# Optimization experiments

Hardware: AMD Instinct MI355X
Metric: run time of the kernel (lower is better)

The kernel has to match this reference:

```python
import jax, jax.numpy as jnp
import numpy as np

B, C, H, W = 32, 512, 32, 32
CI = C // 2  # inter_channels
EPS = 1e-5


def setup_inputs() -> dict:
    key = jax.random.key(0)
    ks = jax.random.split(key, 12)
    s = 0.02
    return {
        "x": jax.random.normal(ks[0], (B, C, H, W), jnp.float32),
        "w_g": jax.random.normal(ks[1], (CI, C), jnp.float32) * s,
        "b_g": jax.random.normal(ks[2], (CI,), jnp.float32) * s,
        "w_theta": jax.random.normal(ks[3], (CI, C), jnp.float32) * s,
        "b_theta": jax.random.normal(ks[4], (CI,), jnp.float32) * s,
        "w_phi": jax.random.normal(ks[5], (CI, C), jnp.float32) * s,
        "b_phi": jax.random.normal(ks[6], (CI,), jnp.float32) * s,
        "w_W": jax.random.normal(ks[7], (C, CI), jnp.float32) * s,
        "b_W": jax.random.normal(ks[8], (C,), jnp.float32) * s,
        "bn_gamma": jax.random.normal(ks[9], (C,), jnp.float32) * 0.1 + 1.0,
        "bn_beta": jax.random.normal(ks[10], (C,), jnp.float32) * 0.1,
        "bn_mean": jax.random.normal(ks[11], (C,), jnp.float32) * 0.1,
        "bn_var": jnp.abs(jax.random.normal(jax.random.fold_in(key, 99), (C,), jnp.float32)) * 0.5 + 0.5,
    }


def reference(x, w_g, b_g, w_theta, b_theta, w_phi, b_phi, w_W, b_W,
              bn_gamma, bn_beta, bn_mean, bn_var):
    b, c, h, w = x.shape
    n = h * w
    xf = x.reshape(b, c, n)  # [B, C, N]
    # 1x1 convs == per-pixel channel matmuls
    g = jnp.einsum('oc,bcn->bon', w_g, xf) + b_g[:, None]          # [B, Ci, N]
    theta = jnp.einsum('oc,bcn->bon', w_theta, xf) + b_theta[:, None]
    phi = jnp.einsum('oc,bcn->bon', w_phi, xf) + b_phi[:, None]
    # f[b, i, j] = theta_i . phi_j ; scaled by 1/N (softmax-free attention)
    f_div_C = jnp.einsum('bcn,bcm->bnm', theta, phi) / n           # [B, N, N]
    # y[b, c, n] = sum_m f[b, n, m] * g[b, c, m]
    y = jnp.einsum('bnm,bcm->bcn', f_div_C, g)                     # [B, Ci, N]
    # W: 1x1 conv back to C channels + BatchNorm (inference form)
    Wy = jnp.einsum('oi,bin->bon', w_W, y) + b_W[:, None]          # [B, C, N]
    inv_std = jax.lax.rsqrt(bn_var + EPS)
    bn = (Wy - bn_mean[:, None]) * (inv_std * bn_gamma)[:, None] + bn_beta[:, None]
    z = bn.reshape(b, c, h, w) + x
    return z
```

## Files before the change

### kernel.cpp

```cpp
#include <hip/hip_runtime.h>
#include <hip/hip_bf16.h>
#include <cstdint>
#include <cstddef>

using bf16 = __hip_bfloat16;
typedef __attribute__((ext_vector_type(8))) short short8v;
typedef __attribute__((ext_vector_type(4))) float f32x4;

static constexpr int BATCH = 32;
static constexpr int CH    = 512;
static constexpr int CIc   = 256;
static constexpr int NSP   = 1024;
#define EPSV 1e-5f

__device__ __forceinline__ bf16 f2bf(float f) { return __float2bfloat16(f); }

__device__ __forceinline__ void gload_lds16(const bf16* g, bf16* l) {
  __builtin_amdgcn_global_load_lds(
      (const __attribute__((address_space(1))) void*)g,
      (__attribute__((address_space(3))) void*)l, 16, 0, 0);
}

__global__ __launch_bounds__(256) void convert_weights(
    const float* __restrict__ wg, const float* __restrict__ wph, const float* __restrict__ wth,
    const float* __restrict__ bg, const float* __restrict__ bph, const float* __restrict__ bth,
    const float* __restrict__ wW,
    bf16* __restrict__ wcat, bf16* __restrict__ wWb, float* __restrict__ biascat)
{
  int i = blockIdx.x * 256 + threadIdx.x;
  const int WSZ = CIc * CH;
  if (i < WSZ) {
    wcat[i]         = f2bf(wg[i]);
    wcat[WSZ + i]   = f2bf(wph[i]);
    wcat[2*WSZ + i] = f2bf(wth[i]);
    wWb[i]          = f2bf(wW[i]);
  }
  if (i < CIc) {
    biascat[i]        = bg[i];
    biascat[CIc + i]  = bph[i];
    biascat[2*CIc + i]= bth[i];
  }
}

__global__ __launch_bounds__(256) void transpose_x_kernel(
    const float* __restrict__ x, bf16* __restrict__ xt)
{
  __shared__ bf16 t[32][34];
  int n0 = blockIdx.x * 32, c0 = blockIdx.y * 32, b = blockIdx.z;
  const float* s = x + (size_t)b * CH * NSP;
  bf16* d = xt + (size_t)b * NSP * CH;
  int tx = threadIdx.x & 31, ty = threadIdx.x >> 5;
  #pragma unroll
  for (int i = 0; i < 32; i += 8)
    t[ty + i][tx] = f2bf(s[(size_t)(c0 + ty + i) * NSP + n0 + tx]);
  __syncthreads();
  #pragma unroll
  for (int i = 0; i < 32; i += 8)
    d[(size_t)(n0 + ty + i) * CH + c0 + tx] = t[tx][ty + i];
}

template<int EPI>
__global__ __launch_bounds__(512, 1) void gemm_nt_256(
    const bf16* __restrict__ A, size_t sA,
    const bf16* __restrict__ Bm, size_t sB,
    void* __restrict__ Cm,
    int K,
    const float* __restrict__ bias,
    bf16* __restrict__ Tt,
    const float* __restrict__ bW, const float* __restrict__ gma,
    const float* __restrict__ bta, const float* __restrict__ mu,
    const float* __restrict__ var,
    const float* __restrict__ xres)
{
  __shared__ bf16 As[2][2][16 * 512];
  __shared__ bf16 Bs[2][2][16 * 512];
  const int zb = blockIdx.z;
  const int m0 = blockIdx.y * 256;
  const int n0 = blockIdx.x * 256;
  const bf16* Ab = A  + (size_t)zb * sA;
  const bf16* Bb = Bm + (size_t)zb * sB;
  const int tid  = threadIdx.x;
  const int wv   = tid >> 6, lane = tid & 63;
  const int l16  = lane & 15, g4 = lane >> 4;
  const int wr   = wv >> 2,  wc = wv & 3;

  f32x4 acc[8][4];
  #pragma unroll
  for (int i = 0; i < 8; ++i)
    #pragma unroll
    for (int j = 0; j < 4; ++j)
      acc[i][j] = (f32x4){0.f, 0.f, 0.f, 0.f};

  auto SH = [&](int tt, int h, int p) {
    int kbase = tt * 64 + h * 32 + g4 * 8;
    #pragma unroll
    for (int q = 0; q < 2; ++q) {
      int f = wv * 2 + q;
      int row = f * 16 + l16;
      gload_lds16(Ab + (size_t)(m0 + row) * K + kbase, &As[p][h][f * 512]);
      gload_lds16(Bb + (size_t)(n0 + row) * K + kbase, &Bs[p][h][f * 512]);
    }
  };

  short8v af[8], bfr[4];
  auto LOADFRAGS = [&](int d, int h) {
    #pragma unroll
    for (int mf = 0; mf < 8; ++mf)
      af[mf] = *(const short8v*)&As[d][h][(wr * 8 + mf) * 512 + lane * 8];
    #pragma unroll
    for (int nf = 0; nf < 4; ++nf)
      bfr[nf] = *(const short8v*)&Bs[d][h][(wc * 4 + nf) * 512 + lane * 8];
  };
  auto MFMAS = [&]() {
    __builtin_amdgcn_s_setprio(1);
    #pragma unroll
    for (int mf = 0; mf < 8; ++mf)
      #pragma unroll
      for (int nf = 0; nf < 4; ++nf)
        acc[mf][nf] = __builtin_amdgcn_mfma_f32_16x16x32_bf16(af[mf], bfr[nf], acc[mf][nf], 0, 0, 0);
    __builtin_amdgcn_s_setprio(0);
  };

  const int nt = K >> 6;
  SH(0, 0, 0); SH(0, 1, 0); SH(1, 0, 1);
  for (int t = 0; t < nt - 1; ++t) {
    const int d = t & 1;
    __builtin_amdgcn_sched_barrier(0);
    asm volatile("s_waitcnt vmcnt(8)" ::: "memory");
    __builtin_amdgcn_s_barrier();
    __builtin_amdgcn_sched_barrier(0);
    LOADFRAGS(d, 0);
    SH(t + 1, 1, d ^ 1);
    MFMAS();
    __builtin_amdgcn_sched_barrier(0);
    asm volatile("s_waitcnt vmcnt(8)" ::: "memory");
    __builtin_amdgcn_s_barrier();
    __builtin_amdgcn_sched_barrier(0);
    LOADFRAGS(d, 1);
    if (t + 2 < nt) SH(t + 2, 0, d);
    MFMAS();
    __builtin_amdgcn_sched_barrier(0);
  }
  {
    const int d = (nt - 1) & 1;
    asm volatile("s_waitcnt vmcnt(4)" ::: "memory");
    __builtin_amdgcn_s_barrier();
    __builtin_amdgcn_sched_barrier(0);
    LOADFRAGS(d, 0);
    MFMAS();
    asm volatile("s_waitcnt vmcnt(0)" ::: "memory");
    __builtin_amdgcn_s_barrier();
    __builtin_amdgcn_sched_barrier(0);
    LOADFRAGS(d, 1);
    MFMAS();
  }

  const int colbase = n0 + wc * 64 + l16;
  const int rowb    = wr * 128 + g4 * 4;

  if constexpr (EPI == 2) {
    #pragma unroll
    for (int mf = 0; mf < 8; ++mf) {
      #pragma unroll
      for (int j = 0; j < 4; ++j) {
        int row = m0 + rowb + mf * 16 + j;
        float a  = gma[row] * rsqrtf(var[row] + EPSV);
        float bb = (bW[row] - mu[row]) * a + bta[row];
        float sc = a * (1.f / (float)NSP);
        #pragma unroll
        for (int nf = 0; nf < 4; ++nf) {
          int col = colbase + nf * 16;
          size_t idx = (size_t)zb * (CH * NSP) + (size_t)row * NSP + col;
          ((float*)Cm)[idx] = acc[mf][nf][j] * sc + bb + ((const float*)xres)[idx];
        }
      }
    }
  } else {
    if (m0 < 512) {
      #pragma unroll
      for (int mf = 0; mf < 8; ++mf)
        #pragma unroll
        for (int j = 0; j < 4; ++j) {
          int row = m0 + rowb + mf * 16 + j;
          float badd = bias[row];
          #pragma unroll
          for (int nf = 0; nf < 4; ++nf) {
            int col = colbase + nf * 16;
            int b = col >> 10, n = col & 1023;
            ((bf16*)Cm)[(size_t)b * (CH * NSP) + (size_t)row * NSP + n] = f2bf(acc[mf][nf][j] + badd);
          }
        }
    } else {
      #pragma unroll
      for (int mf = 0; mf < 8; ++mf) {
        int ci0 = rowb + mf * 16;
        #pragma unroll
        for (int nf = 0; nf < 4; ++nf) {
          int col = colbase + nf * 16;
          int b = col >> 10, n = col & 1023;
          uint64_t pk = 0;
          #pragma unroll
          for (int j = 0; j < 4; ++j) {
            bf16 bv = f2bf(acc[mf][nf][j] + bias[512 + ci0 + j]);
            pk |= (uint64_t)(*(unsigned short*)&bv) << (16 * j);
          }
          *(uint64_t*)(Tt + (size_t)b * (NSP * CIc) + (size_t)n * CIc + ci0) = pk;
        }
      }
    }
  }
}

__global__ __launch_bounds__(256) void gemm_nt_small(
    const bf16* __restrict__ A, size_t sA,
    const bf16* __restrict__ Bm, size_t sB,
    bf16* __restrict__ Cm, size_t sC,
    int N, int K)
{
  __shared__ bf16 As[2][128 * 64];
  __shared__ bf16 Bs[2][128 * 64];
  const int b  = blockIdx.z;
  const int m0 = blockIdx.y * 128;
  const int n0 = blockIdx.x * 128;
  const bf16* Ab = A  + (size_t)b * sA;
  const bf16* Bb = Bm + (size_t)b * sB;
  const int tid  = threadIdx.x;
  const int wv   = tid >> 6, lane = tid & 63;
  const int l16  = lane & 15, g4 = lane >> 4;
  const int wr   = wv >> 1,  wc = wv & 1;

  f32x4 acc[4][4];
  #pragma unroll
  for (int i = 0; i < 4; ++i)
    #pragma unroll
    for (int j = 0; j < 4; ++j)
      acc[i][j] = (f32x4){0.f, 0.f, 0.f, 0.f};

  auto stage = [&](int ks, int p) {
    #pragma unroll
    for (int i = 0; i < 4; ++i) {
      int s = i * 256 + tid;
      int row = s >> 3, ch8 = (s & 7) << 3;
      gload_lds16(Ab + (size_t)(m0 + row) * K + ks + ch8, &As[p][(i * 256 + wv * 64) * 8]);
      gload_lds16(Bb + (size_t)(n0 + row) * K + ks + ch8, &Bs[p][(i * 256 + wv * 64) * 8]);
    }
  };

  const int nt = K >> 6;
  stage(0, 0);
  __syncthreads();
  for (int t = 0; t < nt; ++t) {
    const int cur = t & 1;
    if (t + 1 < nt) stage((t + 1) << 6, cur ^ 1);
    #pragma unroll
    for (int kk = 0; kk < 2; ++kk) {
      short8v af[4], bfv[4];
      #pragma unroll
      for (int mf = 0; mf < 4; ++mf)
        af[mf] = *(const short8v*)&As[cur][(wr * 64 + mf * 16 + l16) * 64 + kk * 32 + g4 * 8];
      #pragma unroll
      for (int nf = 0; nf < 4; ++nf)
        bfv[nf] = *(const short8v*)&Bs[cur][(wc * 64 + nf * 16 + l16) * 64 + kk * 32 + g4 * 8];
      #pragma unroll
      for (int mf = 0; mf < 4; ++mf)
        #pragma unroll
        for (int nf = 0; nf < 4; ++nf)
          acc[mf][nf] = __builtin_amdgcn_mfma_f32_16x16x32_bf16(af[mf], bfv[nf], acc[mf][nf], 0, 0, 0);
    }
    __syncthreads();
  }

  const int colbase = n0 + wc * 64 + l16;
  const int rowbase = m0 + wr * 64 + g4 * 4;
  #pragma unroll
  for (int mf = 0; mf < 4; ++mf)
    #pragma unroll
    for (int j = 0; j < 4; ++j) {
      int row = rowbase + mf * 16 + j;
      #pragma unroll
      for (int nf = 0; nf < 4; ++nf) {
        int col = colbase + nf * 16;
        Cm[(size_t)b * sC + (size_t)row * N + col] = f2bf(acc[mf][nf][j]);
      }
    }
}

extern "C" void kernel_launch(void* const* d_in, const int* in_sizes, int n_in,
                              void* d_out, int out_size, void* d_ws, size_t ws_size,
                              hipStream_t stream)
{
  const float* x    = (const float*)d_in[0];
  const float* w_g  = (const float*)d_in[1];
  const float* b_g  = (const float*)d_in[2];
  const float* w_th = (const float*)d_in[3];
  const float* b_th = (const float*)d_in[4];
  const float* w_ph = (const float*)d_in[5];
  const float* b_ph = (const float*)d_in[6];
  const float* w_W  = (const float*)d_in[7];
  const float* b_W  = (const float*)d_in[8];
  const float* gma  = (const float*)d_in[9];
  const float* bta  = (const float*)d_in[10];
  const float* mu   = (const float*)d_in[11];
  const float* var  = (const float*)d_in[12];
  float* out = (float*)d_out;

  char* ws = (char*)d_ws;
  bf16* proj = (bf16*)(ws + 0);
  bf16* xt   = (bf16*)(ws + 33554432);
  bf16* thT  = (bf16*)(ws + 67108864);
  bf16* S    = (bf16*)(ws + 83886080);
  bf16* T    = (bf16*)(ws + 88080384);
  bf16* wcat = (bf16*)(ws + 96468992);
  bf16* wWb  = (bf16*)(ws + 97255424);
  float* bcat= (float*)(ws + 97517568);

  convert_weights<<<512, 256, 0, stream>>>(w_g, w_ph, w_th, b_g, b_ph, b_th, w_W, wcat, wWb, bcat);
  transpose_x_kernel<<<dim3(32, 16, 32), 256, 0, stream>>>(x, xt);

  gemm_nt_256<1><<<dim3(128, 3, 1), 512, 0, stream>>>(
      wcat, 0, xt, 0, proj, CH, bcat, thT,
      nullptr, nullptr, nullptr, nullptr, nullptr, nullptr);

  gemm_nt_small<<<dim3(2, 2, 32), 256, 0, stream>>>(
      proj + 256 * 1024, (size_t)CH * NSP, proj, (size_t)CH * NSP, S, (size_t)CIc * CIc,
      CIc, NSP);

  gemm_nt_small<<<dim3(2, 4, 32), 256, 0, stream>>>(
      wWb, 0, S, (size_t)CIc * CIc, T, (size_t)CH * CIc,
      CIc, CIc);

  gemm_nt_256<2><<<dim3(4, 2, 32), 512, 0, stream>>>(
      T, (size_t)CH * CIc, thT, (size_t)NSP * CIc, out, CIc,
      nullptr, nullptr, b_W, gma, bta, mu, var, x);
}
```

Before: 139.7 us.

## Shrink GEMM LDS to a 3-stage K=32 ring and allow two blocks per CU

Replaces the 2x2 double-buffered K=64 LDS tiles with a three-stage ring of K=32 slices and raises launch bounds to two blocks per CU. Fragment loads are split into two halves so fewer registers are live, and the next A/B slices are prefetched between the halves. The intent is to raise occupancy so one block's memory latency hides behind another's compute. The cost is twice as many barriers per K, smaller MFMA batches between waits, and tighter register limits that could cause spills.

```diff
diff --git a/kernel.cpp b/kernel.cpp
--- a/kernel.cpp
+++ b/kernel.cpp
@@ -60,7 +60,7 @@
 }
 
 template<int EPI>
-__global__ __launch_bounds__(512, 1) void gemm_nt_256(
+__global__ __launch_bounds__(512, 2) void gemm_nt_256(
     const bf16* __restrict__ A, size_t sA,
     const bf16* __restrict__ Bm, size_t sB,
     void* __restrict__ Cm,
@@ -72,8 +72,8 @@
     const float* __restrict__ var,
     const float* __restrict__ xres)
 {
-  __shared__ bf16 As[2][2][16 * 512];
-  __shared__ bf16 Bs[2][2][16 * 512];
+  __shared__ bf16 As[3][16 * 512];
+  __shared__ bf16 Bs[3][16 * 512];
   const int zb = blockIdx.z;
   const int m0 = blockIdx.y * 256;
   const int n0 = blockIdx.x * 256;
@@ -91,68 +91,70 @@
     for (int j = 0; j < 4; ++j)
       acc[i][j] = (f32x4){0.f, 0.f, 0.f, 0.f};
 
-  auto SH = [&](int tt, int h, int p) {
-    int kbase = tt * 64 + h * 32 + g4 * 8;
+  auto SA = [&](int tt) {
+    int s = tt % 3;
+    int kbase = tt * 32 + g4 * 8;
     #pragma unroll
     for (int q = 0; q < 2; ++q) {
       int f = wv * 2 + q;
-      int row = f * 16 + l16;
-      gload_lds16(Ab + (size_t)(m0 + row) * K + kbase, &As[p][h][f * 512]);
-      gload_lds16(Bb + (size_t)(n0 + row) * K + kbase, &Bs[p][h][f * 512]);
+      gload_lds16(Ab + (size_t)(m0 + f * 16 + l16) * K + kbase, &As[s][f * 512]);
     }
   };
-
-  short8v af[8], bfr[4];
-  auto LOADFRAGS = [&](int d, int h) {
-    #pragma unroll
-    for (int mf = 0; mf < 8; ++mf)
-      af[mf] = *(const short8v*)&As[d][h][(wr * 8 + mf) * 512 + lane * 8];
+  auto SB = [&](int tt) {
+    int s = tt % 3;
+    int kbase = tt * 32 + g4 * 8;
+    #pragma unroll
+    for (int q = 0; q < 2; ++q) {
+      int f = wv * 2 + q;
+      gload_lds16(Bb + (size_t)(n0 + f * 16 + l16) * K + kbase, &Bs[s][f * 512]);
+    }
+  };
+
+  const int nt = K >> 5;
+  SA(0); SB(0); SA(1); SB(1);
+  asm volatile("s_waitcnt vmcnt(4)" ::: "memory");
+  __builtin_amdgcn_s_barrier();
+
+  for (int t = 0; t < nt; ++t) {
+    const int s = t % 3;
+    short8v af[4], bfr[4];
+    #pragma unroll
+    for (int mf = 0; mf < 4; ++mf)
+      af[mf] = *(const short8v*)&As[s][(wr * 8 + mf) * 512 + lane * 8];
     #pragma unroll
     for (int nf = 0; nf < 4; ++nf)
-      bfr[nf] = *(const short8v*)&Bs[d][h][(wc * 4 + nf) * 512 + lane * 8];
-  };
-  auto MFMAS = [&]() {
+      bfr[nf] = *(const short8v*)&Bs[s][(wc * 4 + nf) * 512 + lane * 8];
+    if (t + 2 < nt) SA(t + 2);
+    asm volatile("s_waitcnt lgkmcnt(0)" ::: "memory");
+    __builtin_amdgcn_sched_barrier(0);
     __builtin_amdgcn_s_setprio(1);
     #pragma unroll
-    for (int mf = 0; mf < 8; ++mf)
+    for (int mf = 0; mf < 4; ++mf)
       #pragma unroll
       for (int nf = 0; nf < 4; ++nf)
         acc[mf][nf] = __builtin_amdgcn_mfma_f32_16x16x32_bf16(af[mf], bfr[nf], acc[mf][nf], 0, 0, 0);
     __builtin_amdgcn_s_setprio(0);
-  };
-
-  const int nt = K >> 6;
-  SH(0, 0, 0); SH(0, 1, 0); SH(1, 0, 1);
-  for (int t = 0; t < nt - 1; ++t) {
-    const int d = t & 1;
+
+    short8v af2[4];
+    #pragma unroll
+    for (int mf = 0; mf < 4; ++mf)
+      af2[mf] = *(const short8v*)&As[s][(wr * 8 + 4 + mf) * 512 + lane * 8];
+    if (t + 2 < nt) SB(t + 2);
+    asm volatile("s_waitcnt lgkmcnt(0)" ::: "memory");
     __builtin_amdgcn_sched_barrier(0);
-    asm volatile("s_waitcnt vmcnt(8)" ::: "memory");
-    __builtin_amdgcn_s_barrier();
-    __builtin_amdgcn_sched_barrier(0);
-    LOADFRAGS(d, 0);
-    SH(t + 1, 1, d ^ 1);
-    MFMAS();
-    __builtin_amdgcn_sched_barrier(0);
-    asm volatile("s_waitcnt vmcnt(8)" ::: "memory");
-    __builtin_amdgcn_s_barrier();
-    __builtin_amdgcn_sched_barrier(0);
-    LOADFRAGS(d, 1);
-    if (t + 2 < nt) SH(t + 2, 0, d);
-    MFMAS();
-    __builtin_amdgcn_sched_barrier(0);
-  }
-  {
-    const int d = (nt - 1) & 1;
-    asm volatile("s_waitcnt vmcnt(4)" ::: "memory");
-    __builtin_amdgcn_s_barrier();
-    __builtin_amdgcn_sched_barrier(0);
-    LOADFRAGS(d, 0);
-    MFMAS();
-    asm volatile("s_waitcnt vmcnt(0)" ::: "memory");
-    __builtin_amdgcn_s_barrier();
-    __builtin_amdgcn_sched_barrier(0);
-    LOADFRAGS(d, 1);
-    MFMAS();
+    __builtin_amdgcn_s_setprio(1);
+    #pragma unroll
+    for (int mf = 0; mf < 4; ++mf)
+      #pragma unroll
+      for (int nf = 0; nf < 4; ++nf)
+        acc[4 + mf][nf] = __builtin_amdgcn_mfma_f32_16x16x32_bf16(af2[mf], bfr[nf], acc[4 + mf][nf], 0, 0, 0);
+    __builtin_amdgcn_s_setprio(0);
+
+    if (t + 1 < nt) {
+      if (t + 2 < nt) asm volatile("s_waitcnt vmcnt(4)" ::: "memory");
+      else            asm volatile("s_waitcnt vmcnt(0)" ::: "memory");
+      __builtin_amdgcn_s_barrier();
+    }
   }
 
   const int colbase = n0 + wc * 64 + l16;
```

Result: no change. 141.5 us (+1.3%).
